# Kernel tuning notes

Hardware: AMD Instinct MI355X
Metric: run time of the kernel (lower is better)

Reference implementation:

```python
import jax, jax.numpy as jnp
import numpy as np

N, A, B, K = 100000, 64, 128, 27  # active sites, in/out channels, 3^3 offsets
EPS = 1e-4  # scn BatchNorm default eps
LEAK = 0.0  # leakiness=0 -> ReLU


def bn_lrelu(x, gamma, beta):
    # training-mode BN over active sites, fused leaky relu
    mu = x.mean(0)
    var = x.var(0)
    xh = (x - mu) * jax.lax.rsqrt(var + EPS) * gamma + beta
    return jnp.where(xh > 0, xh, LEAK * xh)


def subconv(f, nbr, mask, W):
    # submanifold conv via rulebook: f [N,Cin], nbr [N,K], mask [N,K], W [K,Cin,Cout]
    out = jnp.zeros((f.shape[0], W.shape[2]), f.dtype)
    for k in range(W.shape[0]):  # fixed small set of kernel offsets
        g = jnp.where(mask[:, k:k + 1], f[nbr[:, k]], jnp.zeros((), f.dtype))
        out = out + g @ W[k]
    return out


def setup_inputs() -> dict:
    key = jax.random.key(0)
    ks = jax.random.split(key, 8)
    feat = jax.random.normal(ks[0], (N, A), jnp.float32)
    nbr = jax.random.randint(ks[1], (N, K), 0, N, jnp.int32)
    mask = jax.random.randint(ks[2], (N, K), 0, 2, jnp.int32).astype(bool)
    # self-connection at center offset is always valid in submanifold conv
    center = K // 2
    nbr = nbr.at[:, center].set(jnp.arange(N, dtype=jnp.int32))
    mask = mask.at[:, center].set(True)
    s1 = 1.0 / np.sqrt(K * A)
    s2 = 1.0 / np.sqrt(K * B)
    W1 = jax.random.normal(ks[3], (K, A, B), jnp.float32) * s1
    W2 = jax.random.normal(ks[4], (K, B, B), jnp.float32) * s2
    Wnin = jax.random.normal(ks[5], (A, B), jnp.float32) / np.sqrt(A)
    gamma1 = jnp.ones((A,), jnp.float32)
    beta1 = jnp.zeros((A,), jnp.float32)
    gamma2 = jnp.ones((B,), jnp.float32)
    beta2 = jnp.zeros((B,), jnp.float32)
    return {"feat": feat, "gamma1": gamma1, "beta1": beta1, "W1": W1,
            "gamma2": gamma2, "beta2": beta2, "W2": W2, "Wnin": Wnin,
            "nbr": nbr, "mask": mask}


def reference(feat, gamma1, beta1, W1, gamma2, beta2, W2, Wnin, nbr, mask):
    y1 = feat @ Wnin  # NetworkInNetwork shortcut (a != b)
    h = bn_lrelu(feat, gamma1, beta1)
    h = subconv(h, nbr, mask, W1)
    h = bn_lrelu(h, gamma2, beta2)
    y2 = subconv(h, nbr, mask, W2)
    return y1 + y2  # add_feature_planes
```

## Files before the change

### kernel.cpp

```cpp
#include <hip/hip_runtime.h>
#include <stdint.h>

#define CA 64
#define CB 128
#define KOFF 27
#define BN_EPS 1e-4f

typedef short bf16x8 __attribute__((ext_vector_type(8)));
typedef float f32x4 __attribute__((ext_vector_type(4)));
typedef unsigned int u32x4 __attribute__((ext_vector_type(4)));
typedef unsigned short u16x4 __attribute__((ext_vector_type(4)));

__device__ __forceinline__ unsigned short f2bf(float f) {
  union { float f; uint32_t u; } c; c.f = f;
  uint32_t u = c.u;
  return (unsigned short)((u + 0x7FFFu + ((u >> 16) & 1u)) >> 16);
}

__device__ __forceinline__ void barrier_lds() {
  asm volatile("s_waitcnt lgkmcnt(0)\n\ts_barrier" ::: "memory");
}

__global__ void detect_mask_k(const unsigned char* __restrict__ m, int* flag) {
  unsigned v = 0;
  for (int i = threadIdx.x; i < 4096; i += 256)
    if (i & 3) v |= m[i];
  if (v) atomicOr(flag, 1);
}

__global__ void make_nbr_eff_k(const int* __restrict__ nbr, const void* __restrict__ mp,
                               const int* __restrict__ flag, int* __restrict__ ne, int n) {
  int i = blockIdx.x * blockDim.x + threadIdx.x;
  if (i >= n * KOFF) return;
  bool m = (*flag) ? (((const unsigned char*)mp)[i] != 0)
                   : (((const int*)mp)[i] != 0);
  ne[i] = m ? nbr[i] : n;
}

__global__ void zero_rows_k(unsigned short* hb1, unsigned short* fb,
                            unsigned short* hb2, int n) {
  int i = threadIdx.x;
  if (i < CA) { hb1[(size_t)n * CA + i] = 0; fb[(size_t)n * CA + i] = 0; }
  if (i < CB) { hb2[(size_t)n * CB + i] = 0; }
}

__global__ void transpose_all_k(const float* __restrict__ W1, const float* __restrict__ W2,
                                const float* __restrict__ Wnin,
                                unsigned short* __restrict__ w1t, unsigned short* __restrict__ w2t,
                                unsigned short* __restrict__ wnt) {
  const int t1 = KOFF * CA * CB, t2 = KOFF * CB * CB, t3 = CA * CB;
  int idx = blockIdx.x * blockDim.x + threadIdx.x;
  if (idx < t1) {
    int ci = idx % CA; int r = idx / CA; int co = r % CB; int k = r / CB;
    w1t[idx] = f2bf(W1[((size_t)k * CA + ci) * CB + co]);
  } else if (idx < t1 + t2) {
    int j = idx - t1;
    int ci = j % CB; int r = j / CB; int co = r % CB; int k = r / CB;
    w2t[j] = f2bf(W2[((size_t)k * CB + ci) * CB + co]);
  } else if (idx < t1 + t2 + t3) {
    int j = idx - t1 - t2;
    int ci = j % CA; int co = j / CA;
    wnt[j] = f2bf(Wnin[(size_t)ci * CB + co]);
  }
}

template<int C>
__global__ void col_stats_k(const float* __restrict__ x, int n, float* __restrict__ sums) {
  __shared__ float ssum[C], ssq[C];
  int t = threadIdx.x;
  for (int i = t; i < C; i += 256) { ssum[i] = 0.f; ssq[i] = 0.f; }
  __syncthreads();
  const int c = t % C;
  const int rpb = 256 / C;
  float s = 0.f, q = 0.f;
  for (int r = blockIdx.x * rpb + t / C; r < n; r += gridDim.x * rpb) {
    float v = x[(size_t)r * C + c];
    s += v; q += v * v;
  }
  atomicAdd(&ssum[c], s);
  atomicAdd(&ssq[c], q);
  __syncthreads();
  for (int i = t; i < C; i += 256) {
    atomicAdd(&sums[i], ssum[i]);
    atomicAdd(&sums[C + i], ssq[i]);
  }
}

template<int C>
__global__ void bn_finalize_k(const float* __restrict__ sums, const float* __restrict__ gamma,
                              const float* __restrict__ beta, float* __restrict__ sc, int n) {
  int c = threadIdx.x;
  if (c >= C) return;
  float inv_n = 1.f / (float)n;
  float mean = sums[c] * inv_n;
  float var = sums[C + c] * inv_n - mean * mean;
  float rstd = rsqrtf(var + BN_EPS);
  float scale = gamma[c] * rstd;
  sc[c] = scale;
  sc[C + c] = beta[c] - mean * scale;
}

template<int C, bool RAW>
__global__ void bn_apply_k(const float* __restrict__ x, const float* __restrict__ sc,
                           unsigned short* __restrict__ h, unsigned short* __restrict__ raw,
                           int total) {
  int idx = (blockIdx.x * blockDim.x + threadIdx.x) * 4;
  if (idx >= total) return;
  f32x4 v = *(const f32x4*)&x[idx];
  int c0 = idx % C;
  u16x4 ho, ro;
#pragma unroll
  for (int j = 0; j < 4; j++) {
    float s = sc[c0 + j], b = sc[C + c0 + j];
    float hv = fmaxf(v[j] * s + b, 0.f);
    ho[j] = f2bf(hv);
    if (RAW) ro[j] = f2bf(v[j]);
  }
  *(u16x4*)&h[idx] = ho;
  if (RAW) *(u16x4*)&raw[idx] = ro;
}

template<int CIN, bool FUSE>
__launch_bounds__(256)
__global__ void conv_k(const unsigned short* __restrict__ hin,
                       const unsigned short* __restrict__ wt,
                       const int* __restrict__ nbr_eff,
                       const unsigned short* __restrict__ fbraw,
                       const unsigned short* __restrict__ wnt,
                       float* __restrict__ out, int n) {
  constexpr int TR = 64;
  constexpr int STR = CIN + 8;
  constexpr int NKS = CIN / 32;
  constexpr int CH = CIN / 8;
  constexpr int NP = TR * CH / 256;

  __shared__ alignas(16) unsigned short tile[2][TR * STR];
  __shared__ int lnbr[TR * KOFF];

  const int t = threadIdx.x;
  const int rowbase = blockIdx.x * TR;
  const int nrows = min(TR, n - rowbase);

  for (int i = t; i < TR * KOFF; i += 256) {
    int r = i / KOFF;
    lnbr[i] = (rowbase + r < n) ? nbr_eff[(size_t)rowbase * KOFF + i] : n;
  }
  __syncthreads();

  const int lane = t & 63;
  const int wave = t >> 6;
  const int l16 = lane & 15;
  const int quad = lane >> 4;
  const int colbase = wave * 32;
  const int goff = (t % CH) * 8;
  const int grow = t / CH;
  const int boff0 = (colbase + l16) * CIN + quad * 8;
  const int boff1 = boff0 + 16 * CIN;

  f32x4 acc[4][2];
#pragma unroll
  for (int i = 0; i < 4; i++) { acc[i][0] = f32x4{0,0,0,0}; acc[i][1] = f32x4{0,0,0,0}; }

  bf16x8 bfr[2][2 * NKS];
  u32x4 gr[4][NP];

#pragma unroll
  for (int j = 0; j < 4; j++) {
#pragma unroll
    for (int p = 0; p < NP; p++) {
      int r = p * (256 / CH) + grow;
      int idx = lnbr[r * KOFF + j];
      gr[j][p] = *(const u32x4*)&hin[(size_t)idx * CIN + goff];
    }
  }
#pragma unroll
  for (int ks = 0; ks < NKS; ks++) {
    bfr[0][2 * ks]     = *(const bf16x8*)&wt[boff0 + ks * 32];
    bfr[0][2 * ks + 1] = *(const bf16x8*)&wt[boff1 + ks * 32];
    const unsigned short* wk = wt + (size_t)CB * CIN;
    bfr[1][2 * ks]     = *(const bf16x8*)&wk[boff0 + ks * 32];
    bfr[1][2 * ks + 1] = *(const bf16x8*)&wk[boff1 + ks * 32];
  }

  if constexpr (FUSE) {
#pragma unroll
    for (int ks = 0; ks < CA / 32; ks++) {
      bf16x8 b0 = *(const bf16x8*)&wnt[(colbase + l16) * CA + ks * 32 + quad * 8];
      bf16x8 b1 = *(const bf16x8*)&wnt[(colbase + 16 + l16) * CA + ks * 32 + quad * 8];
#pragma unroll
      for (int rt = 0; rt < 4; rt++) {
        int g = rowbase + rt * 16 + l16; g = (g < n) ? g : n;
        bf16x8 a = *(const bf16x8*)&fbraw[(size_t)g * CA + ks * 32 + quad * 8];
        acc[rt][0] = __builtin_amdgcn_mfma_f32_16x16x32_bf16(a, b0, acc[rt][0], 0, 0, 0);
        acc[rt][1] = __builtin_amdgcn_mfma_f32_16x16x32_bf16(a, b1, acc[rt][1], 0, 0, 0);
      }
    }
  }

#pragma unroll
  for (int p = 0; p < NP; p++) {
    int r = p * (256 / CH) + grow;
    *(u32x4*)&tile[0][r * STR + goff] = gr[0][p];
  }
  barrier_lds();

#pragma unroll
  for (int k = 0; k < KOFF; k++) {
    const int cur = k & 1;
#pragma unroll
    for (int ks = 0; ks < NKS; ks++) {
#pragma unroll
      for (int rt = 0; rt < 4; rt++) {
        bf16x8 a = *(const bf16x8*)&tile[cur][(rt * 16 + l16) * STR + ks * 32 + quad * 8];
        acc[rt][0] = __builtin_amdgcn_mfma_f32_16x16x32_bf16(a, bfr[cur][2 * ks],     acc[rt][0], 0, 0, 0);
        acc[rt][1] = __builtin_amdgcn_mfma_f32_16x16x32_bf16(a, bfr[cur][2 * ks + 1], acc[rt][1], 0, 0, 0);
      }
    }
    if (k + 4 < KOFF) {
#pragma unroll
      for (int p = 0; p < NP; p++) {
        int r = p * (256 / CH) + grow;
        int idx = lnbr[r * KOFF + (k + 4)];
        gr[(k + 4) & 3][p] = *(const u32x4*)&hin[(size_t)idx * CIN + goff];
      }
    }
    if (k + 2 < KOFF) {
      const unsigned short* wk = wt + (size_t)(k + 2) * CB * CIN;
#pragma unroll
      for (int ks = 0; ks < NKS; ks++) {
        bfr[cur][2 * ks]     = *(const bf16x8*)&wk[boff0 + ks * 32];
        bfr[cur][2 * ks + 1] = *(const bf16x8*)&wk[boff1 + ks * 32];
      }
    }
    if (k + 1 < KOFF) {
#pragma unroll
      for (int p = 0; p < NP; p++) {
        int r = p * (256 / CH) + grow;
        *(u32x4*)&tile[(k + 1) & 1][r * STR + goff] = gr[(k + 1) & 3][p];
      }
      barrier_lds();
    }
  }

#pragma unroll
  for (int rt = 0; rt < 4; rt++) {
#pragma unroll
    for (int ct = 0; ct < 2; ct++) {
#pragma unroll
      for (int i = 0; i < 4; i++) {
        int r = rt * 16 + quad * 4 + i;
        if (r < nrows) {
          int c = colbase + ct * 16 + l16;
          out[(size_t)(rowbase + r) * CB + c] = acc[rt][ct][i];
        }
      }
    }
  }
}

extern "C" void kernel_launch(void* const* d_in, const int* in_sizes, int n_in,
                              void* d_out, int out_size, void* d_ws, size_t ws_size,
                              hipStream_t stream) {
  const float* feat   = (const float*)d_in[0];
  const float* gamma1 = (const float*)d_in[1];
  const float* beta1  = (const float*)d_in[2];
  const float* W1     = (const float*)d_in[3];
  const float* gamma2 = (const float*)d_in[4];
  const float* beta2  = (const float*)d_in[5];
  const float* W2     = (const float*)d_in[6];
  const float* Wnin   = (const float*)d_in[7];
  const int*   nbr    = (const int*)d_in[8];
  const void*  mask   = d_in[9];
  float* out = (float*)d_out;

  const int n = in_sizes[0] / CA;

  char* ws = (char*)d_ws;
  size_t off = 0;
  auto alloc = [&](size_t bytes) { size_t p = off; off += (bytes + 255) & ~(size_t)255; return p; };
  int*            flag  = (int*)           (ws + alloc(256));
  float*          sums1 = (float*)         (ws + alloc(2 * CA * 4));
  float*          sums2 = (float*)         (ws + alloc(2 * CB * 4));
  float*          sc1   = (float*)         (ws + alloc(2 * CA * 4));
  float*          sc2   = (float*)         (ws + alloc(2 * CB * 4));
  int*            neff  = (int*)           (ws + alloc((size_t)n * KOFF * 4));
  unsigned short* fb    = (unsigned short*)(ws + alloc((size_t)(n + 1) * CA * 2));
  unsigned short* hb1   = (unsigned short*)(ws + alloc((size_t)(n + 1) * CA * 2));
  float*          out1  = (float*)         (ws + alloc((size_t)n * CB * 4));
  unsigned short* hb2   = (unsigned short*)(ws + alloc((size_t)(n + 1) * CB * 2));
  unsigned short* w1t   = (unsigned short*)(ws + alloc((size_t)KOFF * CB * CA * 2));
  unsigned short* w2t   = (unsigned short*)(ws + alloc((size_t)KOFF * CB * CB * 2));
  unsigned short* wnt   = (unsigned short*)(ws + alloc((size_t)CB * CA * 2));

  hipMemsetAsync(d_ws, 0, 1792, stream);

  detect_mask_k<<<1, 256, 0, stream>>>((const unsigned char*)mask, flag);
  make_nbr_eff_k<<<(n * KOFF + 255) / 256, 256, 0, stream>>>(nbr, mask, flag, neff, n);
  zero_rows_k<<<1, 256, 0, stream>>>(hb1, fb, hb2, n);

  {
    int tot = KOFF * CA * CB + KOFF * CB * CB + CA * CB;
    transpose_all_k<<<(tot + 255) / 256, 256, 0, stream>>>(W1, W2, Wnin, w1t, w2t, wnt);
  }

  col_stats_k<CA><<<256, 256, 0, stream>>>(feat, n, sums1);
  bn_finalize_k<CA><<<1, CA, 0, stream>>>(sums1, gamma1, beta1, sc1, n);
  bn_apply_k<CA, true><<<(n * CA / 4 + 255) / 256, 256, 0, stream>>>(feat, sc1, hb1, fb, n * CA);

  conv_k<CA, false><<<(n + 63) / 64, 256, 0, stream>>>(hb1, w1t, neff, nullptr, nullptr, out1, n);

  col_stats_k<CB><<<256, 256, 0, stream>>>(out1, n, sums2);
  bn_finalize_k<CB><<<1, CB, 0, stream>>>(sums2, gamma2, beta2, sc2, n);
  bn_apply_k<CB, false><<<(n * CB / 4 + 255) / 256, 256, 0, stream>>>(out1, sc2, hb2, nullptr, n * CB);

  conv_k<CB, true><<<(n + 63) / 64, 256, 0, stream>>>(hb2, w2t, neff, fb, wnt, out, n);
}
```

Baseline: 544.7 us.

## Restructure conv to gather A fragments directly into registers, dropping LDS tiles

The conv kernel no longer stages gathered rows through double-buffered LDS with barriers. Each wave now owns 32 rows and all 128 output columns, and loads the MFMA A fragments straight from global memory via neighbor indices. It uses a 3-deep register pipeline for neighbor indices and A fragments, and double-buffers the B weight fragments. The neighbor table is transposed to offset-major order so per-offset index loads are coalesced, and the launch bounds ask for two blocks per CU. This removes LDS traffic and barrier stalls but raises register pressure, and each wave now reads the full weight slice per offset, so weight traffic from cache grows.

Measured after the change: 989.8 us. 1.82x slower.

```diff
diff --git a/kernel.cpp b/kernel.cpp
--- a/kernel.cpp
+++ b/kernel.cpp
@@ -15,10 +15,6 @@
   union { float f; uint32_t u; } c; c.f = f;
   uint32_t u = c.u;
   return (unsigned short)((u + 0x7FFFu + ((u >> 16) & 1u)) >> 16);
-}
-
-__device__ __forceinline__ void barrier_lds() {
-  asm volatile("s_waitcnt lgkmcnt(0)\n\ts_barrier" ::: "memory");
 }
 
 __global__ void detect_mask_k(const unsigned char* __restrict__ m, int* flag) {
@@ -28,13 +24,15 @@
   if (v) atomicOr(flag, 1);
 }
 
-__global__ void make_nbr_eff_k(const int* __restrict__ nbr, const void* __restrict__ mp,
-                               const int* __restrict__ flag, int* __restrict__ ne, int n) {
-  int i = blockIdx.x * blockDim.x + threadIdx.x;
-  if (i >= n * KOFF) return;
-  bool m = (*flag) ? (((const unsigned char*)mp)[i] != 0)
-                   : (((const int*)mp)[i] != 0);
-  ne[i] = m ? nbr[i] : n;
+__global__ void make_nbrt_k(const int* __restrict__ nbr, const void* __restrict__ mp,
+                            const int* __restrict__ flag, int* __restrict__ nt, int n) {
+  int j = blockIdx.x * blockDim.x + threadIdx.x;
+  if (j >= n * KOFF) return;
+  int k = j / n, row = j - k * n;
+  int src = row * KOFF + k;
+  bool m = (*flag) ? (((const unsigned char*)mp)[src] != 0)
+                   : (((const int*)mp)[src] != 0);
+  nt[j] = m ? nbr[src] : n;
 }
 
 __global__ void zero_rows_k(unsigned short* hb1, unsigned short* fb,
@@ -121,141 +119,102 @@
 }
 
 template<int CIN, bool FUSE>
-__launch_bounds__(256)
+__launch_bounds__(256, 2)
 __global__ void conv_k(const unsigned short* __restrict__ hin,
                        const unsigned short* __restrict__ wt,
-                       const int* __restrict__ nbr_eff,
+                       const int* __restrict__ nbrt,
                        const unsigned short* __restrict__ fbraw,
                        const unsigned short* __restrict__ wnt,
                        float* __restrict__ out, int n) {
-  constexpr int TR = 64;
-  constexpr int STR = CIN + 8;
   constexpr int NKS = CIN / 32;
-  constexpr int CH = CIN / 8;
-  constexpr int NP = TR * CH / 256;
-
-  __shared__ alignas(16) unsigned short tile[2][TR * STR];
-  __shared__ int lnbr[TR * KOFF];
-
   const int t = threadIdx.x;
-  const int rowbase = blockIdx.x * TR;
-  const int nrows = min(TR, n - rowbase);
-
-  for (int i = t; i < TR * KOFF; i += 256) {
-    int r = i / KOFF;
-    lnbr[i] = (rowbase + r < n) ? nbr_eff[(size_t)rowbase * KOFF + i] : n;
-  }
-  __syncthreads();
-
   const int lane = t & 63;
   const int wave = t >> 6;
   const int l16 = lane & 15;
   const int quad = lane >> 4;
-  const int colbase = wave * 32;
-  const int goff = (t % CH) * 8;
-  const int grow = t / CH;
-  const int boff0 = (colbase + l16) * CIN + quad * 8;
-  const int boff1 = boff0 + 16 * CIN;
-
-  f32x4 acc[4][2];
-#pragma unroll
-  for (int i = 0; i < 4; i++) { acc[i][0] = f32x4{0,0,0,0}; acc[i][1] = f32x4{0,0,0,0}; }
-
-  bf16x8 bfr[2][2 * NKS];
-  u32x4 gr[4][NP];
-
-#pragma unroll
-  for (int j = 0; j < 4; j++) {
-#pragma unroll
-    for (int p = 0; p < NP; p++) {
-      int r = p * (256 / CH) + grow;
-      int idx = lnbr[r * KOFF + j];
-      gr[j][p] = *(const u32x4*)&hin[(size_t)idx * CIN + goff];
-    }
-  }
-#pragma unroll
-  for (int ks = 0; ks < NKS; ks++) {
-    bfr[0][2 * ks]     = *(const bf16x8*)&wt[boff0 + ks * 32];
-    bfr[0][2 * ks + 1] = *(const bf16x8*)&wt[boff1 + ks * 32];
-    const unsigned short* wk = wt + (size_t)CB * CIN;
-    bfr[1][2 * ks]     = *(const bf16x8*)&wk[boff0 + ks * 32];
-    bfr[1][2 * ks + 1] = *(const bf16x8*)&wk[boff1 + ks * 32];
-  }
+  const int row0 = blockIdx.x * 128 + wave * 32;
+  const int r0 = row0 + l16;
+  const int r1 = row0 + 16 + l16;
+
+  f32x4 acc[2][8];
+#pragma unroll
+  for (int rt = 0; rt < 2; rt++)
+#pragma unroll
+    for (int ct = 0; ct < 8; ct++) acc[rt][ct] = f32x4{0, 0, 0, 0};
+
+  int nbrv[3][2];
+  bf16x8 A[3][2][NKS];
+  bf16x8 Bb[2][8];
+
+#define LDNBR(K, S) do { \
+    nbrv[S][0] = (r0 < n) ? nbrt[(size_t)(K) * n + r0] : n; \
+    nbrv[S][1] = (r1 < n) ? nbrt[(size_t)(K) * n + r1] : n; } while (0)
+
+#define LDA(S) do { \
+    _Pragma("unroll") \
+    for (int _rt = 0; _rt < 2; _rt++) { \
+      const unsigned short* _rp = hin + (size_t)nbrv[S][_rt] * CIN + quad * 8; \
+      _Pragma("unroll") \
+      for (int _ks = 0; _ks < NKS; _ks++) A[S][_rt][_ks] = *(const bf16x8*)(_rp + _ks * 32); \
+    } } while (0)
+
+#define LDB(K, KS, BUF) do { \
+    const unsigned short* _wp = wt + ((size_t)(K) * CB + l16) * CIN + (KS) * 32 + quad * 8; \
+    _Pragma("unroll") \
+    for (int _ct = 0; _ct < 8; _ct++) Bb[BUF][_ct] = *(const bf16x8*)(_wp + _ct * 16 * CIN); \
+  } while (0)
 
   if constexpr (FUSE) {
+    int rr0 = (r0 < n) ? r0 : n;
+    int rr1 = (r1 < n) ? r1 : n;
 #pragma unroll
     for (int ks = 0; ks < CA / 32; ks++) {
-      bf16x8 b0 = *(const bf16x8*)&wnt[(colbase + l16) * CA + ks * 32 + quad * 8];
-      bf16x8 b1 = *(const bf16x8*)&wnt[(colbase + 16 + l16) * CA + ks * 32 + quad * 8];
-#pragma unroll
-      for (int rt = 0; rt < 4; rt++) {
-        int g = rowbase + rt * 16 + l16; g = (g < n) ? g : n;
-        bf16x8 a = *(const bf16x8*)&fbraw[(size_t)g * CA + ks * 32 + quad * 8];
-        acc[rt][0] = __builtin_amdgcn_mfma_f32_16x16x32_bf16(a, b0, acc[rt][0], 0, 0, 0);
-        acc[rt][1] = __builtin_amdgcn_mfma_f32_16x16x32_bf16(a, b1, acc[rt][1], 0, 0, 0);
+      bf16x8 a0 = *(const bf16x8*)&fbraw[(size_t)rr0 * CA + ks * 32 + quad * 8];
+      bf16x8 a1 = *(const bf16x8*)&fbraw[(size_t)rr1 * CA + ks * 32 + quad * 8];
+#pragma unroll
+      for (int ct = 0; ct < 8; ct++) {
+        bf16x8 b = *(const bf16x8*)&wnt[((size_t)(ct * 16 + l16)) * CA + ks * 32 + quad * 8];
+        acc[0][ct] = __builtin_amdgcn_mfma_f32_16x16x32_bf16(a0, b, acc[0][ct], 0, 0, 0);
+        acc[1][ct] = __builtin_amdgcn_mfma_f32_16x16x32_bf16(a1, b, acc[1][ct], 0, 0, 0);
       }
     }
   }
 
-#pragma unroll
-  for (int p = 0; p < NP; p++) {
-    int r = p * (256 / CH) + grow;
-    *(u32x4*)&tile[0][r * STR + goff] = gr[0][p];
-  }
-  barrier_lds();
-
-#pragma unroll
-  for (int k = 0; k < KOFF; k++) {
-    const int cur = k & 1;
-#pragma unroll
-    for (int ks = 0; ks < NKS; ks++) {
-#pragma unroll
-      for (int rt = 0; rt < 4; rt++) {
-        bf16x8 a = *(const bf16x8*)&tile[cur][(rt * 16 + l16) * STR + ks * 32 + quad * 8];
-        acc[rt][0] = __builtin_amdgcn_mfma_f32_16x16x32_bf16(a, bfr[cur][2 * ks],     acc[rt][0], 0, 0, 0);
-        acc[rt][1] = __builtin_amdgcn_mfma_f32_16x16x32_bf16(a, bfr[cur][2 * ks + 1], acc[rt][1], 0, 0, 0);
-      }
-    }
-    if (k + 4 < KOFF) {
-#pragma unroll
-      for (int p = 0; p < NP; p++) {
-        int r = p * (256 / CH) + grow;
-        int idx = lnbr[r * KOFF + (k + 4)];
-        gr[(k + 4) & 3][p] = *(const u32x4*)&hin[(size_t)idx * CIN + goff];
-      }
-    }
-    if (k + 2 < KOFF) {
-      const unsigned short* wk = wt + (size_t)(k + 2) * CB * CIN;
+  LDNBR(0, 0); LDNBR(1, 1); LDNBR(2, 2);
+  LDA(0); LDA(1);
+  LDB(0, 0, 0);
+
+  for (int kk = 0; kk < KOFF / 3; kk++) {
+#pragma unroll
+    for (int d = 0; d < 3; d++) {
+      const int k = kk * 3 + d;
+      if (k + 3 < KOFF) LDNBR(k + 3, d);
 #pragma unroll
       for (int ks = 0; ks < NKS; ks++) {
-        bfr[cur][2 * ks]     = *(const bf16x8*)&wk[boff0 + ks * 32];
-        bfr[cur][2 * ks + 1] = *(const bf16x8*)&wk[boff1 + ks * 32];
-      }
-    }
-    if (k + 1 < KOFF) {
-#pragma unroll
-      for (int p = 0; p < NP; p++) {
-        int r = p * (256 / CH) + grow;
-        *(u32x4*)&tile[(k + 1) & 1][r * STR + goff] = gr[(k + 1) & 3][p];
-      }
-      barrier_lds();
-    }
-  }
-
-#pragma unroll
-  for (int rt = 0; rt < 4; rt++) {
-#pragma unroll
-    for (int ct = 0; ct < 2; ct++) {
-#pragma unroll
-      for (int i = 0; i < 4; i++) {
-        int r = rt * 16 + quad * 4 + i;
-        if (r < nrows) {
-          int c = colbase + ct * 16 + l16;
-          out[(size_t)(rowbase + r) * CB + c] = acc[rt][ct][i];
+        if (ks + 1 < NKS) LDB(k, ks + 1, (ks + 1) & 1);
+        else if (k + 1 < KOFF) LDB(k + 1, 0, 0);
+        if (ks == 0 && k + 2 < KOFF) LDA((d + 2) % 3);
+#pragma unroll
+        for (int ct = 0; ct < 8; ct++) {
+          acc[0][ct] = __builtin_amdgcn_mfma_f32_16x16x32_bf16(A[d][0][ks], Bb[ks & 1][ct], acc[0][ct], 0, 0, 0);
+          acc[1][ct] = __builtin_amdgcn_mfma_f32_16x16x32_bf16(A[d][1][ks], Bb[ks & 1][ct], acc[1][ct], 0, 0, 0);
         }
       }
     }
   }
+#undef LDNBR
+#undef LDA
+#undef LDB
+
+#pragma unroll
+  for (int rt = 0; rt < 2; rt++)
+#pragma unroll
+    for (int ct = 0; ct < 8; ct++)
+#pragma unroll
+      for (int i = 0; i < 4; i++) {
+        int r = row0 + rt * 16 + quad * 4 + i;
+        if (r < n) out[(size_t)r * CB + ct * 16 + l16] = acc[rt][ct][i];
+      }
 }
 
 extern "C" void kernel_launch(void* const* d_in, const int* in_sizes, int n_in,
@@ -283,7 +242,7 @@
   float*          sums2 = (float*)         (ws + alloc(2 * CB * 4));
   float*          sc1   = (float*)         (ws + alloc(2 * CA * 4));
   float*          sc2   = (float*)         (ws + alloc(2 * CB * 4));
-  int*            neff  = (int*)           (ws + alloc((size_t)n * KOFF * 4));
+  int*            nbrt  = (int*)           (ws + alloc((size_t)n * KOFF * 4));
   unsigned short* fb    = (unsigned short*)(ws + alloc((size_t)(n + 1) * CA * 2));
   unsigned short* hb1   = (unsigned short*)(ws + alloc((size_t)(n + 1) * CA * 2));
   float*          out1  = (float*)         (ws + alloc((size_t)n * CB * 4));
@@ -295,7 +254,7 @@
   hipMemsetAsync(d_ws, 0, 1792, stream);
 
   detect_mask_k<<<1, 256, 0, stream>>>((const unsigned char*)mask, flag);
-  make_nbr_eff_k<<<(n * KOFF + 255) / 256, 256, 0, stream>>>(nbr, mask, flag, neff, n);
+  make_nbrt_k<<<(n * KOFF + 255) / 256, 256, 0, stream>>>(nbr, mask, flag, nbrt, n);
   zero_rows_k<<<1, 256, 0, stream>>>(hb1, fb, hb2, n);
 
   {
@@ -307,11 +266,11 @@
   bn_finalize_k<CA><<<1, CA, 0, stream>>>(sums1, gamma1, beta1, sc1, n);
   bn_apply_k<CA, true><<<(n * CA / 4 + 255) / 256, 256, 0, stream>>>(feat, sc1, hb1, fb, n * CA);
 
-  conv_k<CA, false><<<(n + 63) / 64, 256, 0, stream>>>(hb1, w1t, neff, nullptr, nullptr, out1, n);
+  conv_k<CA, false><<<(n + 127) / 128, 256, 0, stream>>>(hb1, w1t, nbrt, nullptr, nullptr, out1, n);
 
   col_stats_k<CB><<<256, 256, 0, stream>>>(out1, n, sums2);
   bn_finalize_k<CB><<<1, CB, 0, stream>>>(sums2, gamma2, beta2, sc2, n);
   bn_apply_k<CB, false><<<(n * CB / 4 + 255) / 256, 256, 0, stream>>>(out1, sc2, hb2, nullptr, n * CB);
 
-  conv_k<CB, true><<<(n + 63) / 64, 256, 0, stream>>>(hb2, w2t, neff, fb, wnt, out, n);
-}
+  conv_k<CB, true><<<(n + 127) / 128, 256, 0, stream>>>(hb2, w2t, nbrt, fb, wnt, out, n);
+}
```
